# Optimization experiments

Measured on AMD Instinct MI355X. Metric: run time of the kernel, lower is better.

## Reference

```python
import jax, jax.numpy as jnp
import numpy as np
from jax import lax

STRIDE = (1, 1)
PADDING = ((1, 1), (1, 1))
DILATION = (1, 1)


def setup_inputs() -> dict:
    key = jax.random.key(0)
    k1, k2 = jax.random.split(key)
    input = jax.random.normal(k1, (32, 128, 56, 56), dtype=jnp.float32)
    weight = jax.random.normal(k2, (256, 128, 3, 3), dtype=jnp.float32)
    bias = jnp.zeros((256,), dtype=jnp.float32)
    return {"input": input, "weight": weight, "bias": bias}


def reference(input, weight, bias):
    # The original builds the conv's dense matrix via conv2d on an identity
    # basis and then matmuls; that is mathematically identical to a direct
    # conv2d (the map is linear), plus the broadcast bias.
    out = lax.conv_general_dilated(
        input, weight,
        window_strides=STRIDE,
        padding=PADDING,
        rhs_dilation=DILATION,
        dimension_numbers=("NCHW", "OIHW", "NCHW"),
    )
    return out + bias[None, :, None, None]
```

## Files before the change

### kernel.cpp

```cpp
#include <hip/hip_runtime.h>
#include <hip/hip_bf16.h>
#include <stdint.h>


typedef __attribute__((ext_vector_type(8))) short bf16x8;
typedef __attribute__((ext_vector_type(8))) unsigned short ushort8;
typedef __attribute__((ext_vector_type(4))) float f32x4;

#define HW       56
#define SPATIAL  3136
#define C_IN     128
#define K_OUT    256
#define GEMM_K   1152
#define GEMM_N   100352

#define PHW      58
#define PIMG     3364
#define PADTOT_AL 107656

#define BM       256
#define BN       128
#define NTILE    18
#define BUFH     24576

__device__ __forceinline__ unsigned short f2bf(float f) {
    union { float f; unsigned int u; } v; v.f = f;
    unsigned int u = v.u + 0x7FFFu + ((v.u >> 16) & 1u);
    return (unsigned short)(u >> 16);
}

__device__ __forceinline__ void gload16(const unsigned short* g, unsigned short* l) {
    __builtin_amdgcn_global_load_lds(
        (const __attribute__((address_space(1))) unsigned int*)(g),
        (__attribute__((address_space(3))) unsigned int*)(l),
        16, 0, 0);
}

__global__ __launch_bounds__(256)
void prep_all(const float* __restrict__ w, unsigned short* __restrict__ w3,
              const float* __restrict__ in, unsigned short* __restrict__ pad) {
    __shared__ __attribute__((aligned(16))) unsigned short l[56 * 136];
    const int b = blockIdx.x;
    const int tid = threadIdx.x;
    if (b < 1152) {
        int idx = b * 256 + tid;
        int rc   = idx / 18432;
        int rem  = idx % 18432;
        int tap  = rem / 2048;
        int rem2 = rem % 2048;
        int cc   = rem2 / 512;
        int s    = rem2 % 512;
        int li   = s >> 3, j = s & 7;
        int ko   = rc * 16 + (li & 15);
        int c    = cc * 32 + ((li >> 4) << 3) + j;
        w3[idx] = f2bf(w[(ko * C_IN + c) * 9 + tap]);
    } else if (b < 1266) {
        int idx = (b - 1152) * 256 + tid;
        if (idx >= 29184) return;
        int cc  = idx / 7296;
        int r   = idx % 7296;
        int img = r / 228;
        int p   = r % 228;
        int pos;
        if (p < 58)       pos = p;
        else if (p < 116) pos = 57 * PHW + (p - 58);
        else { int i = p - 116; pos = (1 + (i >> 1)) * PHW + (i & 1) * 57; }
        unsigned short* d = pad + (size_t)cc * PADTOT_AL * 32
                          + ((size_t)img * PIMG + pos) * 32;
        const ushort8 z = (ushort8){0,0,0,0,0,0,0,0};
        *reinterpret_cast<ushort8*>(d)      = z;
        *reinterpret_cast<ushort8*>(d + 8)  = z;
        *reinterpret_cast<ushort8*>(d + 16) = z;
        *reinterpret_cast<ushort8*>(d + 24) = z;
    } else {
        const int bx = b - 1266;
        const int n = bx / HW, h = bx % HW;
        const float* src = in + (size_t)n * C_IN * SPATIAL + h * HW;
        #pragma unroll
        for (int i = 0; i < 28; ++i) {
            int idx = i * 256 + tid;
            int c = idx / HW, wv = idx % HW;
            l[wv * 136 + c] = f2bf(src[(size_t)c * SPATIAL + wv]);
        }
        __syncthreads();
        const int prow = n * PIMG + (h + 1) * PHW;
        #pragma unroll
        for (int j = 0; j < 4; ++j) {
            int chunk = j * 256 + tid;
            if (chunk < 896) {
                int wv = chunk >> 4, c8 = chunk & 15;
                int cc = c8 >> 2, sub = c8 & 3;
                unsigned short* dst = pad + (size_t)cc * PADTOT_AL * 32
                                    + (size_t)(prow + wv + 1) * 32 + sub * 8;
                *reinterpret_cast<ushort8*>(dst) =
                    *reinterpret_cast<const ushort8*>(&l[wv * 136 + c8 * 8]);
            }
        }
    }
}

__global__ __launch_bounds__(1024, 1)
void conv_tlp(const unsigned short* __restrict__ pad,
              const unsigned short* __restrict__ w3,
              const float* __restrict__ bias,
              float* __restrict__ out) {
    __shared__ __attribute__((aligned(16))) unsigned short lds[3 * BUFH];

    const int tid  = threadIdx.x;
    const int wave = tid >> 6;
    const int lane = tid & 63;
    const int la   = lane & 15;
    const int lkh  = lane >> 4;

    const int bid = blockIdx.x;
    const int nt  = (bid & 7) * 98 + (bid >> 3);
    const int g0  = nt * BN;

    const int wr = wave >> 2, wc = wave & 3;

    const unsigned short* aw = w3 + (size_t)wave * 18432 + lane * 8;
    const unsigned short* bsrc;
    {
        int col = g0 + (wave >> 1) * 16 + la;
        int img = col / SPATIAL;
        int pos = col - img * SPATIAL;
        int oh  = pos / HW, ow = pos - oh * HW;
        bsrc = pad + (size_t)(img * PIMG + (oh + 1) * PHW + (ow + 1)) * 32 + lkh * 8;
    }
    const int bkc = wave & 1;

    f32x4 acc[4][2];
    #pragma unroll
    for (int i = 0; i < 4; ++i)
        #pragma unroll
        for (int j = 0; j < 2; ++j)
            acc[i][j] = (f32x4){0.f, 0.f, 0.f, 0.f};

    auto STAGE_A0 = [&](int tn) {
        const int tap = tn >> 1, cc = (tn & 1) * 2;
        gload16(aw + (size_t)(tap * 4 + cc) * 512,
                &lds[(tn % 3) * BUFH] + (wave * 2 + 0) * 512);
    };
    auto STAGE_A1 = [&](int tn) {
        const int tap = tn >> 1, cc = (tn & 1) * 2 + 1;
        gload16(aw + (size_t)(tap * 4 + cc) * 512,
                &lds[(tn % 3) * BUFH] + (wave * 2 + 1) * 512);
    };
    auto STAGE_B = [&](int tn) {
        const int tap = tn >> 1, cc = (tn & 1) * 2 + bkc;
        const int dr = tap / 3 - 1, dsx = tap % 3 - 1;
        gload16(bsrc + (size_t)cc * (PADTOT_AL * 32) + (dr * PHW + dsx) * 32,
                &lds[(tn % 3) * BUFH] + 16384 + wave * 512);
    };

    bf16x8 a0[4], b0[2], a1[4], b1[2];

    auto READ0 = [&](int tn, int ks) {
        const unsigned short* Ab = &lds[(tn % 3) * BUFH];
        #pragma unroll
        for (int mi = 0; mi < 4; ++mi)
            a0[mi] = *reinterpret_cast<const bf16x8*>(
                &Ab[((wr * 4 + mi) * 2 + ks) * 512 + lane * 8]);
        #pragma unroll
        for (int nj = 0; nj < 2; ++nj)
            b0[nj] = *reinterpret_cast<const bf16x8*>(
                &Ab[16384 + ((wc * 2 + nj) * 2 + ks) * 512 + lane * 8]);
    };
    auto READ1 = [&](int tn, int ks) {
        const unsigned short* Ab = &lds[(tn % 3) * BUFH];
        #pragma unroll
        for (int mi = 0; mi < 4; ++mi)
            a1[mi] = *reinterpret_cast<const bf16x8*>(
                &Ab[((wr * 4 + mi) * 2 + ks) * 512 + lane * 8]);
        #pragma unroll
        for (int nj = 0; nj < 2; ++nj)
            b1[nj] = *reinterpret_cast<const bf16x8*>(
                &Ab[16384 + ((wc * 2 + nj) * 2 + ks) * 512 + lane * 8]);
    };

    STAGE_A0(0); STAGE_A1(0); STAGE_B(0);
    STAGE_A0(1); STAGE_A1(1); STAGE_B(1);
    asm volatile("s_waitcnt vmcnt(3)" ::: "memory");
    __builtin_amdgcn_s_barrier();
    asm volatile("" ::: "memory");
    READ0(0, 0);

    #pragma unroll
    for (int t = 0; t < NTILE; ++t) {
        READ1(t, 1);
        if (t + 2 < NTILE) { STAGE_A0(t + 2); STAGE_B(t + 2); }
        asm volatile("s_waitcnt lgkmcnt(6)" ::: "memory");
        __builtin_amdgcn_sched_barrier(0);
        __builtin_amdgcn_s_setprio(1);
        #pragma unroll
        for (int mi = 0; mi < 4; ++mi)
            #pragma unroll
            for (int nj = 0; nj < 2; ++nj)
                acc[mi][nj] = __builtin_amdgcn_mfma_f32_16x16x32_bf16(
                    a0[mi], b0[nj], acc[mi][nj], 0, 0, 0);
        __builtin_amdgcn_s_setprio(0);

        if (t + 2 < NTILE) STAGE_A1(t + 2);
        asm volatile("s_waitcnt lgkmcnt(0)" ::: "memory");
        __builtin_amdgcn_sched_barrier(0);
        if (t + 1 < NTILE) {
            if (t + 2 < NTILE)
                asm volatile("s_waitcnt vmcnt(3)" ::: "memory");
            else
                asm volatile("s_waitcnt vmcnt(0)" ::: "memory");
            __builtin_amdgcn_s_barrier();
            asm volatile("" ::: "memory");
            READ0(t + 1, 0);
        }
        __builtin_amdgcn_s_setprio(1);
        #pragma unroll
        for (int mi = 0; mi < 4; ++mi)
            #pragma unroll
            for (int nj = 0; nj < 2; ++nj)
                acc[mi][nj] = __builtin_amdgcn_mfma_f32_16x16x32_bf16(
                    a1[mi], b1[nj], acc[mi][nj], 0, 0, 0);
        __builtin_amdgcn_s_setprio(0);
    }

    #pragma unroll
    for (int mi = 0; mi < 4; ++mi) {
        const int mb = wr * 64 + mi * 16 + lkh * 4;
        const f32x4 bv4 = *reinterpret_cast<const f32x4*>(&bias[mb]);
        #pragma unroll
        for (int nj = 0; nj < 2; ++nj) {
            const int gcol = g0 + wc * 32 + nj * 16;
            const int n2 = gcol / SPATIAL;
            const int p2 = gcol - n2 * SPATIAL + la;
            float* op = out + ((size_t)(n2 * K_OUT + mb)) * SPATIAL + p2;
            op[0]                   = acc[mi][nj][0] + bv4[0];
            op[SPATIAL]             = acc[mi][nj][1] + bv4[1];
            op[2 * SPATIAL]         = acc[mi][nj][2] + bv4[2];
            op[3 * (size_t)SPATIAL] = acc[mi][nj][3] + bv4[3];
        }
    }
}

#define LDK 40
__global__ __launch_bounds__(256)
void conv_mfma_fallback(const float* __restrict__ in,
                        const float* __restrict__ wraw,
                        const float* __restrict__ bias,
                        float* __restrict__ out) {
    __shared__ __attribute__((aligned(16))) unsigned short lA[128 * LDK];
    __shared__ __attribute__((aligned(16))) unsigned short lB[128 * LDK];
    const int tid = threadIdx.x;
    const int m0  = blockIdx.y * 128;
    const int g0  = blockIdx.x * 128;
    const int wave = tid >> 6, lane = tid & 63;
    const int wr = wave >> 1, wc = wave & 1;
    const int la = lane & 15, lkh = lane >> 4, lk = lkh * 8;

    f32x4 acc[4][4];
    #pragma unroll
    for (int i = 0; i < 4; ++i)
        #pragma unroll
        for (int j = 0; j < 4; ++j)
            acc[i][j] = (f32x4){0.f, 0.f, 0.f, 0.f};

    const int jj = tid & 127;
    const int kb = (tid >> 7) * 16;
    const int g = g0 + jj;
    const int nimg = g / SPATIAL;
    const int pos  = g % SPATIAL;
    const int oh = pos / HW, ow = pos % HW;

    for (int tap = 0; tap < 9; ++tap) {
        const int dr = tap / 3 - 1, dsx = tap % 3 - 1;
        const int ih = oh + dr, iw = ow + dsx;
        const bool valid = ((unsigned)ih < HW) && ((unsigned)iw < HW);
        const float* src = in + ((nimg * C_IN) * HW + ih) * HW + iw;
        for (int c0 = 0; c0 < C_IN; c0 += 32) {
            #pragma unroll
            for (int i = 0; i < 2; ++i) {
                const int ch = tid * 2 + i;
                const int row = ch >> 2;
                const int kp = (ch & 3) * 8;
                ushort8 v;
                #pragma unroll
                for (int e = 0; e < 8; ++e)
                    v[e] = f2bf(wraw[((m0 + row) * C_IN + c0 + kp + e) * 9 + tap]);
                *reinterpret_cast<ushort8*>(&lA[row * LDK + kp]) = v;
            }
            {
                ushort8 v0, v1;
                #pragma unroll
                for (int i = 0; i < 8; ++i)
                    v0[i] = f2bf(valid ? src[(c0 + kb + i) * SPATIAL] : 0.f);
                #pragma unroll
                for (int i = 0; i < 8; ++i)
                    v1[i] = f2bf(valid ? src[(c0 + kb + 8 + i) * SPATIAL] : 0.f);
                *reinterpret_cast<ushort8*>(&lB[jj * LDK + kb])     = v0;
                *reinterpret_cast<ushort8*>(&lB[jj * LDK + kb + 8]) = v1;
            }
            __syncthreads();
            bf16x8 af[4], bv[4];
            #pragma unroll
            for (int f = 0; f < 4; ++f) {
                af[f] = *reinterpret_cast<const bf16x8*>(&lA[(wr * 64 + f * 16 + la) * LDK + lk]);
                bv[f] = *reinterpret_cast<const bf16x8*>(&lB[(wc * 64 + f * 16 + la) * LDK + lk]);
            }
            #pragma unroll
            for (int fi = 0; fi < 4; ++fi)
                #pragma unroll
                for (int fj = 0; fj < 4; ++fj)
                    acc[fi][fj] = __builtin_amdgcn_mfma_f32_16x16x32_bf16(
                        af[fi], bv[fj], acc[fi][fj], 0, 0, 0);
            __syncthreads();
        }
    }
    const int mbase = m0 + wr * 64;
    const int cbase = g0 + wc * 64;
    #pragma unroll
    for (int fi = 0; fi < 4; ++fi) {
        float bvv[4];
        #pragma unroll
        for (int r = 0; r < 4; ++r)
            bvv[r] = bias[mbase + fi * 16 + lkh * 4 + r];
        #pragma unroll
        for (int fj = 0; fj < 4; ++fj) {
            const int gcol = cbase + fj * 16 + la;
            const int n2 = gcol / SPATIAL;
            const int p2 = gcol % SPATIAL;
            float* op = out + (size_t)(n2 * K_OUT) * SPATIAL + p2;
            #pragma unroll
            for (int r = 0; r < 4; ++r)
                op[(size_t)(mbase + fi * 16 + lkh * 4 + r) * SPATIAL] = acc[fi][fj][r] + bvv[r];
        }
    }
}

extern "C" void kernel_launch(void* const* d_in, const int* in_sizes, int n_in,
                              void* d_out, int out_size, void* d_ws, size_t ws_size,
                              hipStream_t stream) {
    const float* in   = (const float*)d_in[0];
    const float* w    = (const float*)d_in[1];
    const float* bias = (const float*)d_in[2];
    float* out = (float*)d_out;

    const size_t pad_halves = 4ull * PADTOT_AL * 32ull;
    const size_t need_bytes = (pad_halves + 294912ull) * 2ull;

    if (ws_size >= need_bytes) {
        unsigned short* pad = (unsigned short*)d_ws;
        unsigned short* w3  = pad + pad_halves;
        prep_all<<<1266 + 32 * HW, 256, 0, stream>>>(w, w3, in, pad);
        conv_tlp<<<GEMM_N / BN, 1024, 0, stream>>>(pad, w3, bias, out);
    } else {
        dim3 grid(GEMM_N / 128, K_OUT / 128);
        conv_mfma_fallback<<<grid, 256, 0, stream>>>(in, w, bias, out);
    }
}
```

Baseline: 92.30 us.

## Halve K-step per stage and LDS footprint to fit two blocks per CU

Restructures the conv GEMM main loop from 18 tiles of K=64 into 36 tiles of K=32. Each stage is now one A load per wave, plus one B load on the first 8 waves only. The triple LDS buffer shrinks to half its size, and the launch bound hint changes from 1 to 8, so more blocks can be resident per CU and latency can be hidden across blocks. In exchange the loop runs twice as many barriers and waitcnts. The old split that overlapped reading the second K-half from LDS with MFMAs on the first half is removed, and every MFMA group now waits for all LDS reads first.

```diff
diff --git a/kernel.cpp b/kernel.cpp
--- a/kernel.cpp
+++ b/kernel.cpp
@@ -20,8 +20,8 @@
 
 #define BM       256
 #define BN       128
-#define NTILE    18
-#define BUFH     24576
+#define NT32     36
+#define BUFH     12288
 
 __device__ __forceinline__ unsigned short f2bf(float f) {
     union { float f; unsigned int u; } v; v.f = f;
@@ -99,11 +99,11 @@
     }
 }
 
-__global__ __launch_bounds__(1024, 1)
-void conv_tlp(const unsigned short* __restrict__ pad,
-              const unsigned short* __restrict__ w3,
-              const float* __restrict__ bias,
-              float* __restrict__ out) {
+__global__ __launch_bounds__(1024, 8)
+void conv_tlp8(const unsigned short* __restrict__ pad,
+               const unsigned short* __restrict__ w3,
+               const float* __restrict__ bias,
+               float* __restrict__ out) {
     __shared__ __attribute__((aligned(16))) unsigned short lds[3 * BUFH];
 
     const int tid  = threadIdx.x;
@@ -121,13 +121,13 @@
     const unsigned short* aw = w3 + (size_t)wave * 18432 + lane * 8;
     const unsigned short* bsrc;
     {
-        int col = g0 + (wave >> 1) * 16 + la;
+        int col = g0 + (wave & 7) * 16 + la;
         int img = col / SPATIAL;
         int pos = col - img * SPATIAL;
         int oh  = pos / HW, ow = pos - oh * HW;
         bsrc = pad + (size_t)(img * PIMG + (oh + 1) * PHW + (ow + 1)) * 32 + lkh * 8;
     }
-    const int bkc = wave & 1;
+    const bool stagesB = (wave < 8);
 
     f32x4 acc[4][2];
     #pragma unroll
@@ -136,60 +136,42 @@
         for (int j = 0; j < 2; ++j)
             acc[i][j] = (f32x4){0.f, 0.f, 0.f, 0.f};
 
-    auto STAGE_A0 = [&](int tn) {
-        const int tap = tn >> 1, cc = (tn & 1) * 2;
-        gload16(aw + (size_t)(tap * 4 + cc) * 512,
-                &lds[(tn % 3) * BUFH] + (wave * 2 + 0) * 512);
+    auto STAGE = [&](int tn) {
+        const int tap = tn >> 2, cc = tn & 3;
+        const int dr = tap / 3 - 1, dsx = tap % 3 - 1;
+        unsigned short* dst = &lds[(tn % 3) * BUFH];
+        gload16(aw + (size_t)(tap * 4 + cc) * 512, dst + wave * 512);
+        if (stagesB)
+            gload16(bsrc + (size_t)cc * (PADTOT_AL * 32) + (dr * PHW + dsx) * 32,
+                    dst + 8192 + wave * 512);
     };
-    auto STAGE_A1 = [&](int tn) {
-        const int tap = tn >> 1, cc = (tn & 1) * 2 + 1;
-        gload16(aw + (size_t)(tap * 4 + cc) * 512,
-                &lds[(tn % 3) * BUFH] + (wave * 2 + 1) * 512);
+
+    bf16x8 a[4], b[2];
+
+    auto READF = [&](int tn) {
+        const unsigned short* Ab = &lds[(tn % 3) * BUFH];
+        #pragma unroll
+        for (int mi = 0; mi < 4; ++mi)
+            a[mi] = *reinterpret_cast<const bf16x8*>(
+                &Ab[(wr * 4 + mi) * 512 + lane * 8]);
+        #pragma unroll
+        for (int nj = 0; nj < 2; ++nj)
+            b[nj] = *reinterpret_cast<const bf16x8*>(
+                &Ab[8192 + (wc * 2 + nj) * 512 + lane * 8]);
     };
-    auto STAGE_B = [&](int tn) {
-        const int tap = tn >> 1, cc = (tn & 1) * 2 + bkc;
-        const int dr = tap / 3 - 1, dsx = tap % 3 - 1;
-        gload16(bsrc + (size_t)cc * (PADTOT_AL * 32) + (dr * PHW + dsx) * 32,
-                &lds[(tn % 3) * BUFH] + 16384 + wave * 512);
-    };
-
-    bf16x8 a0[4], b0[2], a1[4], b1[2];
-
-    auto READ0 = [&](int tn, int ks) {
-        const unsigned short* Ab = &lds[(tn % 3) * BUFH];
-        #pragma unroll
-        for (int mi = 0; mi < 4; ++mi)
-            a0[mi] = *reinterpret_cast<const bf16x8*>(
-                &Ab[((wr * 4 + mi) * 2 + ks) * 512 + lane * 8]);
-        #pragma unroll
-        for (int nj = 0; nj < 2; ++nj)
-            b0[nj] = *reinterpret_cast<const bf16x8*>(
-                &Ab[16384 + ((wc * 2 + nj) * 2 + ks) * 512 + lane * 8]);
-    };
-    auto READ1 = [&](int tn, int ks) {
-        const unsigned short* Ab = &lds[(tn % 3) * BUFH];
-        #pragma unroll
-        for (int mi = 0; mi < 4; ++mi)
-            a1[mi] = *reinterpret_cast<const bf16x8*>(
-                &Ab[((wr * 4 + mi) * 2 + ks) * 512 + lane * 8]);
-        #pragma unroll
-        for (int nj = 0; nj < 2; ++nj)
-            b1[nj] = *reinterpret_cast<const bf16x8*>(
-                &Ab[16384 + ((wc * 2 + nj) * 2 + ks) * 512 + lane * 8]);
-    };
-
-    STAGE_A0(0); STAGE_A1(0); STAGE_B(0);
-    STAGE_A0(1); STAGE_A1(1); STAGE_B(1);
-    asm volatile("s_waitcnt vmcnt(3)" ::: "memory");
+
+    STAGE(0); STAGE(1);
+    if (stagesB) asm volatile("s_waitcnt vmcnt(2)" ::: "memory");
+    else         asm volatile("s_waitcnt vmcnt(1)" ::: "memory");
     __builtin_amdgcn_s_barrier();
     asm volatile("" ::: "memory");
-    READ0(0, 0);
-
-    #pragma unroll
-    for (int t = 0; t < NTILE; ++t) {
-        READ1(t, 1);
-        if (t + 2 < NTILE) { STAGE_A0(t + 2); STAGE_B(t + 2); }
-        asm volatile("s_waitcnt lgkmcnt(6)" ::: "memory");
+    READF(0);
+
+    #pragma unroll
+    for (int t = 0; t < NT32; ++t) {
+        if (t + 2 < NT32) STAGE(t + 2);
+
+        asm volatile("s_waitcnt lgkmcnt(0)" ::: "memory");
         __builtin_amdgcn_sched_barrier(0);
         __builtin_amdgcn_s_setprio(1);
         #pragma unroll
@@ -197,29 +179,20 @@
             #pragma unroll
             for (int nj = 0; nj < 2; ++nj)
                 acc[mi][nj] = __builtin_amdgcn_mfma_f32_16x16x32_bf16(
-                    a0[mi], b0[nj], acc[mi][nj], 0, 0, 0);
+                    a[mi], b[nj], acc[mi][nj], 0, 0, 0);
         __builtin_amdgcn_s_setprio(0);
 
-        if (t + 2 < NTILE) STAGE_A1(t + 2);
-        asm volatile("s_waitcnt lgkmcnt(0)" ::: "memory");
-        __builtin_amdgcn_sched_barrier(0);
-        if (t + 1 < NTILE) {
-            if (t + 2 < NTILE)
-                asm volatile("s_waitcnt vmcnt(3)" ::: "memory");
-            else
+        if (t + 1 < NT32) {
+            if (t + 2 < NT32) {
+                if (stagesB) asm volatile("s_waitcnt vmcnt(2)" ::: "memory");
+                else         asm volatile("s_waitcnt vmcnt(1)" ::: "memory");
+            } else {
                 asm volatile("s_waitcnt vmcnt(0)" ::: "memory");
+            }
             __builtin_amdgcn_s_barrier();
             asm volatile("" ::: "memory");
-            READ0(t + 1, 0);
-        }
-        __builtin_amdgcn_s_setprio(1);
-        #pragma unroll
-        for (int mi = 0; mi < 4; ++mi)
-            #pragma unroll
-            for (int nj = 0; nj < 2; ++nj)
-                acc[mi][nj] = __builtin_amdgcn_mfma_f32_16x16x32_bf16(
-                    a1[mi], b1[nj], acc[mi][nj], 0, 0, 0);
-        __builtin_amdgcn_s_setprio(0);
+            READF(t + 1);
+        }
     }
 
     #pragma unroll
@@ -349,7 +322,7 @@
         unsigned short* pad = (unsigned short*)d_ws;
         unsigned short* w3  = pad + pad_halves;
         prep_all<<<1266 + 32 * HW, 256, 0, stream>>>(w, w3, in, pad);
-        conv_tlp<<<GEMM_N / BN, 1024, 0, stream>>>(pad, w3, bias, out);
+        conv_tlp8<<<GEMM_N / BN, 1024, 0, stream>>>(pad, w3, bias, out);
     } else {
         dim3 grid(GEMM_N / 128, K_OUT / 128);
         conv_mfma_fallback<<<grid, 256, 0, stream>>>(in, w, bias, out);
```

After: 122.2 us. +32.4%, slower.

## Switch conv GEMM to 32x32x16 MFMA with 256-column tiles

Applied to the files above, without the earlier changes.

Replaces the 16x16x32 bf16 MFMA tiling with 32x32x16 MFMA, doubling the N tile to 256 columns and halving the K step per stage (36 stages of 32 channels instead of 18 of 64). The weight pre-pack layout changes to match the 32-row MFMA operand format. Larger MFMA tiles raise arithmetic per LDS read and halve the grid size. The tradeoffs are more pipeline stages and barriers, fewer blocks per CU, and a scattered epilogue store pattern with per-element bias loads.

```diff
diff --git a/kernel.cpp b/kernel.cpp
--- a/kernel.cpp
+++ b/kernel.cpp
@@ -6,6 +6,7 @@
 typedef __attribute__((ext_vector_type(8))) short bf16x8;
 typedef __attribute__((ext_vector_type(8))) unsigned short ushort8;
 typedef __attribute__((ext_vector_type(4))) float f32x4;
+typedef __attribute__((ext_vector_type(16))) float f32x16;
 
 #define HW       56
 #define SPATIAL  3136
@@ -18,10 +19,9 @@
 #define PIMG     3364
 #define PADTOT_AL 107656
 
-#define BM       256
-#define BN       128
-#define NTILE    18
-#define BUFH     24576
+#define BN       256
+#define NTILE    36
+#define BUFM     16384
 
 __device__ __forceinline__ unsigned short f2bf(float f) {
     union { float f; unsigned int u; } v; v.f = f;
@@ -44,15 +44,15 @@
     const int tid = threadIdx.x;
     if (b < 1152) {
         int idx = b * 256 + tid;
-        int rc   = idx / 18432;
-        int rem  = idx % 18432;
-        int tap  = rem / 2048;
-        int rem2 = rem % 2048;
-        int cc   = rem2 / 512;
+        int rc8  = idx / 36864;
+        int rem  = idx % 36864;
+        int tap  = rem / 4096;
+        int rem2 = rem % 4096;
+        int kc   = rem2 / 512;
         int s    = rem2 % 512;
         int li   = s >> 3, j = s & 7;
-        int ko   = rc * 16 + (li & 15);
-        int c    = cc * 32 + ((li >> 4) << 3) + j;
+        int ko   = rc8 * 32 + (li & 31);
+        int c    = kc * 16 + ((li >> 5) << 3) + j;
         w3[idx] = f2bf(w[(ko * C_IN + c) * 9 + tap]);
     } else if (b < 1266) {
         int idx = (b - 1152) * 256 + tid;
@@ -100,87 +100,82 @@
 }
 
 __global__ __launch_bounds__(1024, 1)
-void conv_tlp(const unsigned short* __restrict__ pad,
+void conv_m32(const unsigned short* __restrict__ pad,
               const unsigned short* __restrict__ w3,
               const float* __restrict__ bias,
               float* __restrict__ out) {
-    __shared__ __attribute__((aligned(16))) unsigned short lds[3 * BUFH];
+    __shared__ __attribute__((aligned(16))) unsigned short lds[3 * BUFM];
 
     const int tid  = threadIdx.x;
     const int wave = tid >> 6;
     const int lane = tid & 63;
-    const int la   = lane & 15;
-    const int lkh  = lane >> 4;
+    const int l31  = lane & 31;
+    const int lhi  = lane >> 5;
 
     const int bid = blockIdx.x;
-    const int nt  = (bid & 7) * 98 + (bid >> 3);
+    const int nt  = (bid & 7) * 49 + (bid >> 3);
     const int g0  = nt * BN;
 
     const int wr = wave >> 2, wc = wave & 3;
 
-    const unsigned short* aw = w3 + (size_t)wave * 18432 + lane * 8;
+    const unsigned short* aw = w3 + (size_t)(wave >> 1) * 36864 + lane * 8;
     const unsigned short* bsrc;
     {
-        int col = g0 + (wave >> 1) * 16 + la;
+        int col = g0 + (wave >> 1) * 32 + l31;
         int img = col / SPATIAL;
         int pos = col - img * SPATIAL;
         int oh  = pos / HW, ow = pos - oh * HW;
-        bsrc = pad + (size_t)(img * PIMG + (oh + 1) * PHW + (ow + 1)) * 32 + lkh * 8;
-    }
-    const int bkc = wave & 1;
-
-    f32x4 acc[4][2];
-    #pragma unroll
-    for (int i = 0; i < 4; ++i)
+        bsrc = pad + (size_t)(img * PIMG + (oh + 1) * PHW + (ow + 1)) * 32
+             + (wave & 1) * 16 + (lhi << 3);
+    }
+    const int wks = wave & 1;
+
+    f32x16 acc[2][2];
+    #pragma unroll
+    for (int i = 0; i < 2; ++i)
         #pragma unroll
         for (int j = 0; j < 2; ++j)
-            acc[i][j] = (f32x4){0.f, 0.f, 0.f, 0.f};
-
-    auto STAGE_A0 = [&](int tn) {
-        const int tap = tn >> 1, cc = (tn & 1) * 2;
-        gload16(aw + (size_t)(tap * 4 + cc) * 512,
-                &lds[(tn % 3) * BUFH] + (wave * 2 + 0) * 512);
+            #pragma unroll
+            for (int r = 0; r < 16; ++r)
+                acc[i][j][r] = 0.f;
+
+    auto STAGE = [&](int tn) {
+        const int tap = tn >> 2, cc32 = tn & 3;
+        const int kc  = cc32 * 2 + wks;
+        const int dr = tap / 3 - 1, dsx = tap % 3 - 1;
+        unsigned short* dst = &lds[(tn % 3) * BUFM];
+        gload16(aw + (size_t)(tap * 8 + kc) * 512, dst + wave * 512);
+        gload16(bsrc + (size_t)cc32 * (PADTOT_AL * 32) + (dr * PHW + dsx) * 32,
+                dst + 8192 + wave * 512);
     };
-    auto STAGE_A1 = [&](int tn) {
-        const int tap = tn >> 1, cc = (tn & 1) * 2 + 1;
-        gload16(aw + (size_t)(tap * 4 + cc) * 512,
-                &lds[(tn % 3) * BUFH] + (wave * 2 + 1) * 512);
-    };
-    auto STAGE_B = [&](int tn) {
-        const int tap = tn >> 1, cc = (tn & 1) * 2 + bkc;
-        const int dr = tap / 3 - 1, dsx = tap % 3 - 1;
-        gload16(bsrc + (size_t)cc * (PADTOT_AL * 32) + (dr * PHW + dsx) * 32,
-                &lds[(tn % 3) * BUFH] + 16384 + wave * 512);
-    };
-
-    bf16x8 a0[4], b0[2], a1[4], b1[2];
+
+    bf16x8 a0[2], b0[2], a1[2], b1[2];
 
     auto READ0 = [&](int tn, int ks) {
-        const unsigned short* Ab = &lds[(tn % 3) * BUFH];
-        #pragma unroll
-        for (int mi = 0; mi < 4; ++mi)
+        const unsigned short* Ab = &lds[(tn % 3) * BUFM];
+        #pragma unroll
+        for (int mi = 0; mi < 2; ++mi)
             a0[mi] = *reinterpret_cast<const bf16x8*>(
-                &Ab[((wr * 4 + mi) * 2 + ks) * 512 + lane * 8]);
+                &Ab[((wr * 2 + mi) * 2 + ks) * 512 + lane * 8]);
         #pragma unroll
         for (int nj = 0; nj < 2; ++nj)
             b0[nj] = *reinterpret_cast<const bf16x8*>(
-                &Ab[16384 + ((wc * 2 + nj) * 2 + ks) * 512 + lane * 8]);
+                &Ab[8192 + ((wc * 2 + nj) * 2 + ks) * 512 + lane * 8]);
     };
     auto READ1 = [&](int tn, int ks) {
-        const unsigned short* Ab = &lds[(tn % 3) * BUFH];
-        #pragma unroll
-        for (int mi = 0; mi < 4; ++mi)
+        const unsigned short* Ab = &lds[(tn % 3) * BUFM];
+        #pragma unroll
+        for (int mi = 0; mi < 2; ++mi)
             a1[mi] = *reinterpret_cast<const bf16x8*>(
-                &Ab[((wr * 4 + mi) * 2 + ks) * 512 + lane * 8]);
+                &Ab[((wr * 2 + mi) * 2 + ks) * 512 + lane * 8]);
         #pragma unroll
         for (int nj = 0; nj < 2; ++nj)
             b1[nj] = *reinterpret_cast<const bf16x8*>(
-                &Ab[16384 + ((wc * 2 + nj) * 2 + ks) * 512 + lane * 8]);
+                &Ab[8192 + ((wc * 2 + nj) * 2 + ks) * 512 + lane * 8]);
     };
 
-    STAGE_A0(0); STAGE_A1(0); STAGE_B(0);
-    STAGE_A0(1); STAGE_A1(1); STAGE_B(1);
-    asm volatile("s_waitcnt vmcnt(3)" ::: "memory");
+    STAGE(0); STAGE(1);
+    asm volatile("s_waitcnt vmcnt(2)" ::: "memory");
     __builtin_amdgcn_s_barrier();
     asm volatile("" ::: "memory");
     READ0(0, 0);
@@ -188,24 +183,23 @@
     #pragma unroll
     for (int t = 0; t < NTILE; ++t) {
         READ1(t, 1);
-        if (t + 2 < NTILE) { STAGE_A0(t + 2); STAGE_B(t + 2); }
-        asm volatile("s_waitcnt lgkmcnt(6)" ::: "memory");
+        if (t + 2 < NTILE) STAGE(t + 2);
+        asm volatile("s_waitcnt lgkmcnt(4)" ::: "memory");
         __builtin_amdgcn_sched_barrier(0);
         __builtin_amdgcn_s_setprio(1);
         #pragma unroll
-        for (int mi = 0; mi < 4; ++mi)
+        for (int mi = 0; mi < 2; ++mi)
             #pragma unroll
             for (int nj = 0; nj < 2; ++nj)
-                acc[mi][nj] = __builtin_amdgcn_mfma_f32_16x16x32_bf16(
+                acc[mi][nj] = __builtin_amdgcn_mfma_f32_32x32x16_bf16(
                     a0[mi], b0[nj], acc[mi][nj], 0, 0, 0);
         __builtin_amdgcn_s_setprio(0);
 
-        if (t + 2 < NTILE) STAGE_A1(t + 2);
         asm volatile("s_waitcnt lgkmcnt(0)" ::: "memory");
         __builtin_amdgcn_sched_barrier(0);
         if (t + 1 < NTILE) {
             if (t + 2 < NTILE)
-                asm volatile("s_waitcnt vmcnt(3)" ::: "memory");
+                asm volatile("s_waitcnt vmcnt(2)" ::: "memory");
             else
                 asm volatile("s_waitcnt vmcnt(0)" ::: "memory");
             __builtin_amdgcn_s_barrier();
@@ -214,28 +208,28 @@
         }
         __builtin_amdgcn_s_setprio(1);
         #pragma unroll
-        for (int mi = 0; mi < 4; ++mi)
+        for (int mi = 0; mi < 2; ++mi)
             #pragma unroll
             for (int nj = 0; nj < 2; ++nj)
-                acc[mi][nj] = __builtin_amdgcn_mfma_f32_16x16x32_bf16(
+                acc[mi][nj] = __builtin_amdgcn_mfma_f32_32x32x16_bf16(
                     a1[mi], b1[nj], acc[mi][nj], 0, 0, 0);
         __builtin_amdgcn_s_setprio(0);
     }
 
     #pragma unroll
-    for (int mi = 0; mi < 4; ++mi) {
-        const int mb = wr * 64 + mi * 16 + lkh * 4;
-        const f32x4 bv4 = *reinterpret_cast<const f32x4*>(&bias[mb]);
+    for (int mi = 0; mi < 2; ++mi) {
+        const int mbase = wr * 64 + mi * 32 + (lhi << 2);
         #pragma unroll
         for (int nj = 0; nj < 2; ++nj) {
-            const int gcol = g0 + wc * 32 + nj * 16;
+            const int gcol = g0 + wc * 64 + nj * 32 + l31;
             const int n2 = gcol / SPATIAL;
-            const int p2 = gcol - n2 * SPATIAL + la;
-            float* op = out + ((size_t)(n2 * K_OUT + mb)) * SPATIAL + p2;
-            op[0]                   = acc[mi][nj][0] + bv4[0];
-            op[SPATIAL]             = acc[mi][nj][1] + bv4[1];
-            op[2 * SPATIAL]         = acc[mi][nj][2] + bv4[2];
-            op[3 * (size_t)SPATIAL] = acc[mi][nj][3] + bv4[3];
+            const int p2 = gcol - n2 * SPATIAL;
+            float* op = out + ((size_t)(n2 * K_OUT + mbase)) * SPATIAL + p2;
+            #pragma unroll
+            for (int r = 0; r < 16; ++r) {
+                const int ro = (r & 3) + 8 * (r >> 2);
+                op[(size_t)ro * SPATIAL] = acc[mi][nj][r] + bias[mbase + ro];
+            }
         }
     }
 }
@@ -349,7 +343,7 @@
         unsigned short* pad = (unsigned short*)d_ws;
         unsigned short* w3  = pad + pad_halves;
         prep_all<<<1266 + 32 * HW, 256, 0, stream>>>(w, w3, in, pad);
-        conv_tlp<<<GEMM_N / BN, 1024, 0, stream>>>(pad, w3, bias, out);
+        conv_m32<<<GEMM_N / BN, 1024, 0, stream>>>(pad, w3, bias, out);
     } else {
         dim3 grid(GEMM_N / 128, K_OUT / 128);
         conv_mfma_fallback<<<grid, 256, 0, stream>>>(in, w, bias, out);
```

Result: no change. 93.09 us (+0.8%).
